# Performance work log

Hardware: AMD Instinct MI355X
Metric: run time of the kernel (lower is better)

## Reference

```python
import jax, jax.numpy as jnp
import numpy as np

UNITS = 512

def gru_cell(x, h, W, U, b):
    # Keras GRUCell, reset_after=True (v2 / cuDNN-compatible formulation)
    # x: [B, D], h: [B, U], W: [D, 3U], U: [U, 3U], b: [2, 3U]
    bi, br = b[0], b[1]
    xg = x @ W + bi          # input gates  [B, 3U]
    hg = h @ U + br          # recurrent gates [B, 3U]
    xz, xr, xh = jnp.split(xg, 3, axis=-1)
    hz, hr, hh = jnp.split(hg, 3, axis=-1)
    z = jax.nn.sigmoid(xz + hz)
    r = jax.nn.sigmoid(xr + hr)
    cand = jnp.tanh(xh + r * hh)
    return z * h + (1.0 - z) * cand

def setup_inputs() -> dict:
    key = jax.random.key(0)
    ks = jax.random.split(key, 7)
    B, T, D, U = 64, 1024, 512, UNITS
    s_in = 1.0 / np.sqrt(D)
    s_rec = 1.0 / np.sqrt(U)
    return {
        "x":  jax.random.normal(ks[0], (B, T, D), dtype=jnp.float32),
        "W0": jax.random.normal(ks[1], (D, 3 * U), dtype=jnp.float32) * s_in,
        "U0": jax.random.normal(ks[2], (U, 3 * U), dtype=jnp.float32) * s_rec,
        "b0": jax.random.normal(ks[3], (2, 3 * U), dtype=jnp.float32) * 0.01,
        "W1": jax.random.normal(ks[4], (U, 3 * U), dtype=jnp.float32) * s_rec,
        "U1": jax.random.normal(ks[5], (U, 3 * U), dtype=jnp.float32) * s_rec,
        "b1": jax.random.normal(ks[6], (2, 3 * U), dtype=jnp.float32) * 0.01,
    }

def reference(x, W0, U0, b0, W1, U1, b1):
    B = x.shape[0]
    h0_init = jnp.zeros((B, UNITS), dtype=x.dtype)
    h1_init = jnp.zeros((B, UNITS), dtype=x.dtype)

    def step(carry, x_t):
        h0, h1 = carry
        h0 = gru_cell(x_t, h0, W0, U0, b0)   # cell 0 consumes input
        h1 = gru_cell(h0, h1, W1, U1, b1)    # cell 1 consumes cell 0 output
        return (h0, h1), None

    xs = jnp.swapaxes(x, 0, 1)  # [T, B, D] for scan over time
    (h0, h1), _ = jax.lax.scan(step, (h0_init, h1_init), xs)
    # RNN(return_sequences=False) returns last-step output of last cell
    return h1
```

## Files before the change

kernel.cpp:

```cpp
#include <hip/hip_runtime.h>


typedef __bf16 bf16x8 __attribute__((ext_vector_type(8)));
typedef float  f32x4  __attribute__((ext_vector_type(4)));
typedef unsigned int uint4v __attribute__((ext_vector_type(4)));

#define T_STEPS 1024
#define NWG 256
#define NTHR 256
#define SMEM_BYTES (98304 + 4096 + 1024 + 128 + 16)

__device__ __align__(16) unsigned int g_h0[1025LL * 64 * 512];
__device__ __align__(16) unsigned int g_h1[1025LL * 64 * 512];
__device__ unsigned int g_leaf[8 * 64];
__device__ unsigned int g_root[64];
__device__ unsigned int g_epoch[64];
__device__ __align__(256) unsigned int g_flag[2][2][8][64];

__device__ __forceinline__ void f2hilo(float f, unsigned short& hi, unsigned short& lo) {
    __bf16 h = (__bf16)f;
    float  fh = (float)h;
    __bf16 l = (__bf16)(f - fh);
    hi = __builtin_bit_cast(unsigned short, h);
    lo = __builtin_bit_cast(unsigned short, l);
}

__device__ __forceinline__ f32x4 mfma16(bf16x8 a, bf16x8 b, f32x4 c) {
    return __builtin_amdgcn_mfma_f32_16x16x32_bf16(a, b, c, 0, 0, 0);
}

__device__ __forceinline__ void unpack8(const unsigned int* p, bf16x8& ah, bf16x8& al) {
    uint4v v0 = *(const uint4v*)p;
    uint4v v1 = *(const uint4v*)(p + 4);
    uint4v h, l;
    h.x = __builtin_amdgcn_perm(v0.y, v0.x, 0x07060302u);
    h.y = __builtin_amdgcn_perm(v0.w, v0.z, 0x07060302u);
    h.z = __builtin_amdgcn_perm(v1.y, v1.x, 0x07060302u);
    h.w = __builtin_amdgcn_perm(v1.w, v1.z, 0x07060302u);
    l.x = __builtin_amdgcn_perm(v0.y, v0.x, 0x05040100u);
    l.y = __builtin_amdgcn_perm(v0.w, v0.z, 0x05040100u);
    l.z = __builtin_amdgcn_perm(v1.y, v1.x, 0x05040100u);
    l.w = __builtin_amdgcn_perm(v1.w, v1.z, 0x05040100u);
    ah = __builtin_bit_cast(bf16x8, h);
    al = __builtin_bit_cast(bf16x8, l);
}

__device__ __forceinline__ void cvt8(const float* p, bf16x8& ah, bf16x8& al) {
    float4 a = *(const float4*)p;
    float4 b = *(const float4*)(p + 4);
    float f[8] = {a.x, a.y, a.z, a.w, b.x, b.y, b.z, b.w};
    bf16x8 h, l;
    #pragma unroll
    for (int i = 0; i < 8; ++i) {
        __bf16 hv = (__bf16)f[i];
        h[i] = hv;
        l[i] = (__bf16)(f[i] - (float)hv);
    }
    ah = h; al = l;
}

__device__ __forceinline__ void gemm_pass(
    bool useX, int pass, int ntile, int lane, int lcol, int kch,
    const float* A0x, const unsigned int* Ap,
    const unsigned short* sBhi, const unsigned short* sBlo,
    f32x4& acc_zr, f32x4& acc_xh, f32x4& acc_hh)
{
    bf16x8 bzero = {};
    if (ntile == 0) {
        #pragma unroll 4
        for (int ks = 0; ks < 16; ++ks) {
            bf16x8 ah, al;
            if (useX) cvt8(A0x + ks * 32 + kch * 8, ah, al);
            else      unpack8(Ap + ks * 32 + kch * 8, ah, al);
            const int o = pass * 12288 + ks * 512 + lane * 8;
            bf16x8 bh = *(const bf16x8*)(sBhi + o);
            bf16x8 bl = *(const bf16x8*)(sBlo + o);
            acc_zr = mfma16(ah, bh, acc_zr);
            acc_zr = mfma16(ah, bl, acc_zr);
            acc_zr = mfma16(al, bh, acc_zr);
        }
    } else {
        #pragma unroll 4
        for (int ks = 0; ks < 16; ++ks) {
            bf16x8 ah, al;
            if (useX) cvt8(A0x + ks * 32 + kch * 8, ah, al);
            else      unpack8(Ap + ks * 32 + kch * 8, ah, al);
            bf16x8 bh = bzero, bl = bzero;
            if (lcol < 8) {
                const int e = kch * 8 + lcol;
                const int o = pass * 12288 + 8192 + ks * 256 + e * 8;
                bh = *(const bf16x8*)(sBhi + o);
                bl = *(const bf16x8*)(sBlo + o);
            }
            f32x4 acc = pass ? acc_hh : acc_xh;
            acc = mfma16(ah, bh, acc);
            acc = mfma16(ah, bl, acc);
            acc = mfma16(al, bh, acc);
            if (pass) acc_hh = acc; else acc_xh = acc;
        }
    }
}

__device__ __forceinline__ float epilogue_hn(
    int tid, int mtile, int ntile, int lane, int lcol,
    const f32x4& acc_zr, const f32x4& acc_xh, const f32x4& acc_hh,
    float* sAcc, float* sHprev, const float* sBias)
{
    const int drow = mtile * 16 + (lane >> 4) * 4;
    if (ntile == 0) {
        #pragma unroll
        for (int r2 = 0; r2 < 4; ++r2) sAcc[(drow + r2) * 16 + lcol] = acc_zr[r2];
    } else if (lcol < 8) {
        #pragma unroll
        for (int r2 = 0; r2 < 4; ++r2) {
            sAcc[512 + (drow + r2) * 8 + lcol] = acc_xh[r2];
            sAcc[768 + (drow + r2) * 8 + lcol] = acc_hh[r2];
        }
    }
    __syncthreads();
    const int ml  = tid >> 3;
    const int col = tid & 7;
    const float zp = sAcc[ml * 16 + col]     + sBias[col];
    const float rp = sAcc[ml * 16 + 8 + col] + sBias[8 + col];
    const float z = 1.f / (1.f + __expf(-zp));
    const float r = 1.f / (1.f + __expf(-rp));
    const float xh = sAcc[512 + ml * 8 + col] + sBias[16 + col];
    const float hh = sAcc[768 + ml * 8 + col] + sBias[24 + col];
    const float ct = tanhf(xh + r * hh);
    const float hp = sHprev[tid];
    const float hn = z * hp + (1.f - z) * ct;
    sHprev[tid] = hn;
    return hn;
}

__device__ __forceinline__ void wait_one(const unsigned int* P, unsigned int target, int tid) {
    if (tid < 64) {
        while (true) {
            unsigned int v = __hip_atomic_load(P + tid, __ATOMIC_RELAXED,
                                               __HIP_MEMORY_SCOPE_AGENT);
            if (__ballot(v >= target) == ~0ull) break;
            __builtin_amdgcn_s_sleep(1);
        }
    }
    __syncthreads();
}

__device__ __forceinline__ void wait_two(const unsigned int* Pa, unsigned int ta,
                                         const unsigned int* Pb, unsigned int tb, int tid) {
    if (tid < 64) {
        bool da = false, db = false;
        while (true) {
            if (!da) {
                unsigned int v = __hip_atomic_load(Pa + tid, __ATOMIC_RELAXED,
                                                   __HIP_MEMORY_SCOPE_AGENT);
                da = (__ballot(v >= ta) == ~0ull);
            }
            if (!db) {
                unsigned int v = __hip_atomic_load(Pb + tid, __ATOMIC_RELAXED,
                                                   __HIP_MEMORY_SCOPE_AGENT);
                db = (__ballot(v >= tb) == ~0ull);
            }
            if (da && db) break;
            __builtin_amdgcn_s_sleep(1);
        }
    }
    __syncthreads();
}

__global__ void __launch_bounds__(NTHR, 1) gru_persistent(
    const float* __restrict__ x,  const float* __restrict__ W0,
    const float* __restrict__ U0, const float* __restrict__ b0,
    const float* __restrict__ W1, const float* __restrict__ U1,
    const float* __restrict__ b1, float* __restrict__ out)
{
    extern __shared__ char smem[];
    unsigned short* sBhi = (unsigned short*)smem;
    unsigned short* sBlo = sBhi + 24576;
    float* sAcc   = (float*)(smem + 98304);
    float* sHprev = sAcc + 1024;
    float* sBias  = sHprev + 256;
    unsigned int* sE0 = (unsigned int*)(sBias + 32);

    const int wg    = blockIdx.x;
    const int g     = wg >> 7;
    const int cell  = (wg >> 6) & 1;
    const int slice = wg & 63;
    const int c0    = slice * 8;
    const int tid   = threadIdx.x;

    __builtin_amdgcn_fence(__ATOMIC_ACQUIRE, "agent");

    if (tid == 0)
        sE0[0] = __hip_atomic_load(&g_epoch[0], __ATOMIC_RELAXED, __HIP_MEMORY_SCOPE_AGENT);

    {
        const int ml = tid >> 3, col = tid & 7;
        unsigned int* dst = (cell ? g_h1 : g_h0)
                          + (long long)(g * 32 + ml) * 512 + (c0 + col);
        __hip_atomic_store(dst, 0u, __ATOMIC_RELAXED, __HIP_MEMORY_SCOPE_AGENT);
    }
    if (tid < 8) {
        unsigned int* f = &g_flag[0][0][0][0];
        __hip_atomic_store(f + wg * 8 + tid, 0u, __ATOMIC_RELAXED, __HIP_MEMORY_SCOPE_AGENT);
    }

    {
        const float* Wm = cell ? W1 : W0;
        const float* Um = cell ? U1 : U0;
        for (int e = tid; e < 24576; e += NTHR) {
            const int pass = e / 12288;
            const int rem  = e % 12288;
            int j, gcol;
            if (rem < 8192) {
                const int ks = rem >> 9, r2 = rem & 511;
                const int entry = r2 >> 3, i = r2 & 7;
                const int col = entry & 15, kch = entry >> 4;
                j = ks * 32 + kch * 8 + i;
                gcol = (col < 8) ? (c0 + col) : (512 + c0 + col - 8);
            } else {
                const int r2 = rem - 8192;
                const int ks = r2 >> 8, r3 = r2 & 255;
                const int entry = r3 >> 3, i = r3 & 7;
                const int col = entry & 7, kch = entry >> 3;
                j = ks * 32 + kch * 8 + i;
                gcol = 1024 + c0 + col;
            }
            const float v = (pass ? Um : Wm)[j * 1536 + gcol];
            f2hilo(v, sBhi[e], sBlo[e]);
        }
    }
    {
        const float* b = cell ? b1 : b0;
        if (tid < 32) {
            const int col = tid & 7, sec = tid >> 3;
            float v;
            if (sec == 0)      v = b[c0 + col] + b[1536 + c0 + col];
            else if (sec == 1) v = b[512 + c0 + col] + b[1536 + 512 + c0 + col];
            else if (sec == 2) v = b[1024 + c0 + col];
            else               v = b[1536 + 1024 + c0 + col];
            sBias[tid] = v;
        }
        sHprev[tid] = 0.f;
    }
    __syncthreads();
    const unsigned int E0 = sE0[0];

    {
        const unsigned int target = E0 + 1u;
        if (tid == 0) {
            asm volatile("s_waitcnt vmcnt(0)" ::: "memory");
            unsigned int o = __hip_atomic_fetch_add(&g_leaf[(wg & 7) * 64], 1u,
                                __ATOMIC_RELAXED, __HIP_MEMORY_SCOPE_AGENT);
            if (o == 32u * target - 1u) {
                unsigned int r = __hip_atomic_fetch_add(&g_root[0], 1u,
                                    __ATOMIC_RELAXED, __HIP_MEMORY_SCOPE_AGENT);
                if (r == 8u * target - 1u)
                    __hip_atomic_store(&g_epoch[0], target,
                                       __ATOMIC_RELAXED, __HIP_MEMORY_SCOPE_AGENT);
            }
        }
        while ((int)(__hip_atomic_load(&g_epoch[0], __ATOMIC_RELAXED,
                                       __HIP_MEMORY_SCOPE_AGENT) - target) < 0)
            __builtin_amdgcn_s_sleep(1);
        asm volatile("" ::: "memory");
        __syncthreads();
    }

    const int lane  = tid & 63;
    const int mtile = (tid >> 6) & 1;
    const int ntile = tid >> 7;
    const int lcol  = lane & 15;
    const int kch   = lane >> 4;
    const int arow  = g * 32 + mtile * 16 + lcol;

    if (cell == 0) {
        unsigned int* const myflag = &g_flag[0][g][0][0];
        for (int k = 0; k < T_STEPS; ++k) {
            f32x4 acc_zr = {0.f, 0.f, 0.f, 0.f};
            f32x4 acc_xh = {0.f, 0.f, 0.f, 0.f};
            f32x4 acc_hh = {0.f, 0.f, 0.f, 0.f};
            const float* A0x = x + ((long long)arow * 1024 + k) * 512;
            gemm_pass(true, 0, ntile, lane, lcol, kch, A0x, nullptr,
                      sBhi, sBlo, acc_zr, acc_xh, acc_hh);

            if (k > 0)
                wait_one(&g_flag[0][g][(k - 1) & 7][0], (unsigned int)k, tid);

            const unsigned int* A1p = g_h0 + ((long long)k * (64 * 512)) + arow * 512;
            gemm_pass(false, 1, ntile, lane, lcol, kch, nullptr, A1p,
                      sBhi, sBlo, acc_zr, acc_xh, acc_hh);

            const float hn = epilogue_hn(tid, mtile, ntile, lane, lcol,
                                         acc_zr, acc_xh, acc_hh, sAcc, sHprev, sBias);
            {
                const int ml = tid >> 3, col = tid & 7;
                unsigned short hi_, lo_;
                f2hilo(hn, hi_, lo_);
                const unsigned int pk = ((unsigned int)hi_ << 16) | (unsigned int)lo_;
                unsigned int* dst = g_h0 + (long long)(k + 1) * (64 * 512)
                                  + (long long)(g * 32 + ml) * 512 + (c0 + col);
                __hip_atomic_store(dst, pk, __ATOMIC_RELAXED, __HIP_MEMORY_SCOPE_AGENT);
            }
            __syncthreads();
            if (tid == 0)
                __hip_atomic_store(myflag + ((k & 7) * 64) + slice, (unsigned int)(k + 1),
                                   __ATOMIC_RELAXED, __HIP_MEMORY_SCOPE_AGENT);
        }
    } else {
        unsigned int* const myflag = &g_flag[1][g][0][0];
        for (int t = 0; t < T_STEPS; ++t) {
            if (t > 0)
                wait_two(&g_flag[1][g][(t - 1) & 7][0], (unsigned int)t,
                         &g_flag[0][g][t & 7][0], (unsigned int)(t + 1), tid);
            else
                wait_one(&g_flag[0][g][0][0], 1u, tid);

            f32x4 acc_zr = {0.f, 0.f, 0.f, 0.f};
            f32x4 acc_xh = {0.f, 0.f, 0.f, 0.f};
            f32x4 acc_hh = {0.f, 0.f, 0.f, 0.f};
            const unsigned int* A0p = g_h0 + ((long long)(t + 1) * (64 * 512)) + arow * 512;
            const unsigned int* A1p = g_h1 + ((long long)t * (64 * 512)) + arow * 512;
            gemm_pass(false, 0, ntile, lane, lcol, kch, nullptr, A0p,
                      sBhi, sBlo, acc_zr, acc_xh, acc_hh);
            gemm_pass(false, 1, ntile, lane, lcol, kch, nullptr, A1p,
                      sBhi, sBlo, acc_zr, acc_xh, acc_hh);

            const float hn = epilogue_hn(tid, mtile, ntile, lane, lcol,
                                         acc_zr, acc_xh, acc_hh, sAcc, sHprev, sBias);
            {
                const int ml = tid >> 3, col = tid & 7;
                unsigned short hi_, lo_;
                f2hilo(hn, hi_, lo_);
                const unsigned int pk = ((unsigned int)hi_ << 16) | (unsigned int)lo_;
                unsigned int* dst = g_h1 + (long long)(t + 1) * (64 * 512)
                                  + (long long)(g * 32 + ml) * 512 + (c0 + col);
                __hip_atomic_store(dst, pk, __ATOMIC_RELAXED, __HIP_MEMORY_SCOPE_AGENT);
                if (t == T_STEPS - 1)
                    out[(g * 32 + ml) * 512 + (c0 + col)] = hn;
            }
            __syncthreads();
            if (tid == 0)
                __hip_atomic_store(myflag + ((t & 7) * 64) + slice, (unsigned int)(t + 1),
                                   __ATOMIC_RELAXED, __HIP_MEMORY_SCOPE_AGENT);
        }
    }
}

extern "C" void kernel_launch(void* const* d_in, const int* in_sizes, int n_in,
                              void* d_out, int out_size, void* d_ws, size_t ws_size,
                              hipStream_t stream) {
    (void)in_sizes; (void)n_in; (void)d_ws; (void)ws_size; (void)out_size;
    const float* x  = (const float*)d_in[0];
    const float* W0 = (const float*)d_in[1];
    const float* U0 = (const float*)d_in[2];
    const float* b0 = (const float*)d_in[3];
    const float* W1 = (const float*)d_in[4];
    const float* U1 = (const float*)d_in[5];
    const float* b1 = (const float*)d_in[6];
    float* out = (float*)d_out;

    hipFuncSetAttribute((const void*)gru_persistent,
                        hipFuncAttributeMaxDynamicSharedMemorySize, SMEM_BYTES);
    void* args[] = {&x, &W0, &U0, &b0, &W1, &U1, &b1, &out};
    hipLaunchCooperativeKernel((const void*)gru_persistent, dim3(NWG), dim3(NTHR),
                               args, SMEM_BYTES, stream);
}
```

Before: 10.70 ms.

## Replace per-slice flag polling with monotonic counters and overlap cell1 recurrent GEMM

Each slice used to publish its own step flag in a ring buffer, and waiters polled all 64 flags with a wavefront ballot. Now each slice does one atomic increment on a shared per-group counter per step, and one thread polls a single word with sleep backoff. Counters are never reset; each launch reads them at startup and uses that value as its baseline. Cell 1 now runs its recurrent GEMM on its own previous state before waiting on cell 0's current output, so that work overlaps with cell 0, at the cost of 64-way atomic contention on one address.

```diff
diff --git a/kernel.cpp b/kernel.cpp
--- a/kernel.cpp
+++ b/kernel.cpp
@@ -8,14 +8,15 @@
 #define T_STEPS 1024
 #define NWG 256
 #define NTHR 256
-#define SMEM_BYTES (98304 + 4096 + 1024 + 128 + 16)
+#define SMEM_BYTES (98304 + 4096 + 1024 + 128 + 32)
 
 __device__ __align__(16) unsigned int g_h0[1025LL * 64 * 512];
 __device__ __align__(16) unsigned int g_h1[1025LL * 64 * 512];
 __device__ unsigned int g_leaf[8 * 64];
 __device__ unsigned int g_root[64];
 __device__ unsigned int g_epoch[64];
-__device__ __align__(256) unsigned int g_flag[2][2][8][64];
+__device__ __align__(256) unsigned int g_cnt[2][2][64];
+__device__ __align__(256) unsigned int g_cntx[2][64];
 
 __device__ __forceinline__ void f2hilo(float f, unsigned short& hi, unsigned short& lo) {
     __bf16 h = (__bf16)f;
@@ -133,35 +134,14 @@
     return hn;
 }
 
-__device__ __forceinline__ void wait_one(const unsigned int* P, unsigned int target, int tid) {
-    if (tid < 64) {
-        while (true) {
-            unsigned int v = __hip_atomic_load(P + tid, __ATOMIC_RELAXED,
-                                               __HIP_MEMORY_SCOPE_AGENT);
-            if (__ballot(v >= target) == ~0ull) break;
-            __builtin_amdgcn_s_sleep(1);
-        }
-    }
-    __syncthreads();
-}
-
-__device__ __forceinline__ void wait_two(const unsigned int* Pa, unsigned int ta,
-                                         const unsigned int* Pb, unsigned int tb, int tid) {
-    if (tid < 64) {
-        bool da = false, db = false;
-        while (true) {
-            if (!da) {
-                unsigned int v = __hip_atomic_load(Pa + tid, __ATOMIC_RELAXED,
-                                                   __HIP_MEMORY_SCOPE_AGENT);
-                da = (__ballot(v >= ta) == ~0ull);
-            }
-            if (!db) {
-                unsigned int v = __hip_atomic_load(Pb + tid, __ATOMIC_RELAXED,
-                                                   __HIP_MEMORY_SCOPE_AGENT);
-                db = (__ballot(v >= tb) == ~0ull);
-            }
-            if (da && db) break;
-            __builtin_amdgcn_s_sleep(1);
+__device__ __forceinline__ void wait_cnt(unsigned int* C, unsigned int target, int tid) {
+    if (tid == 0) {
+        int spins = 0;
+        while ((int)(__hip_atomic_load(C, __ATOMIC_RELAXED,
+                                       __HIP_MEMORY_SCOPE_AGENT) - target) < 0) {
+            if (spins < 4) __builtin_amdgcn_s_sleep(1);
+            else           __builtin_amdgcn_s_sleep(8);
+            ++spins;
         }
     }
     __syncthreads();
@@ -190,18 +170,17 @@
 
     __builtin_amdgcn_fence(__ATOMIC_ACQUIRE, "agent");
 
-    if (tid == 0)
+    if (tid == 0) {
         sE0[0] = __hip_atomic_load(&g_epoch[0], __ATOMIC_RELAXED, __HIP_MEMORY_SCOPE_AGENT);
+        sE0[1] = __hip_atomic_load(&g_cnt[cell][g][0], __ATOMIC_RELAXED, __HIP_MEMORY_SCOPE_AGENT);
+        sE0[2] = __hip_atomic_load(&g_cntx[g][0], __ATOMIC_RELAXED, __HIP_MEMORY_SCOPE_AGENT);
+    }
 
     {
         const int ml = tid >> 3, col = tid & 7;
         unsigned int* dst = (cell ? g_h1 : g_h0)
                           + (long long)(g * 32 + ml) * 512 + (c0 + col);
         __hip_atomic_store(dst, 0u, __ATOMIC_RELAXED, __HIP_MEMORY_SCOPE_AGENT);
-    }
-    if (tid < 8) {
-        unsigned int* f = &g_flag[0][0][0][0];
-        __hip_atomic_store(f + wg * 8 + tid, 0u, __ATOMIC_RELAXED, __HIP_MEMORY_SCOPE_AGENT);
     }
 
     {
@@ -243,7 +222,9 @@
         sHprev[tid] = 0.f;
     }
     __syncthreads();
-    const unsigned int E0 = sE0[0];
+    const unsigned int E0     = sE0[0];
+    const unsigned int Cown   = sE0[1];
+    const unsigned int Ccross = sE0[2];
 
     {
         const unsigned int target = E0 + 1u;
@@ -272,9 +253,12 @@
     const int lcol  = lane & 15;
     const int kch   = lane >> 4;
     const int arow  = g * 32 + mtile * 16 + lcol;
+    const int ml    = tid >> 3;
+    const int colw  = tid & 7;
 
     if (cell == 0) {
-        unsigned int* const myflag = &g_flag[0][g][0][0];
+        unsigned int* const cnt  = &g_cnt[0][g][0];
+        unsigned int* const cntx = &g_cntx[g][0];
         for (int k = 0; k < T_STEPS; ++k) {
             f32x4 acc_zr = {0.f, 0.f, 0.f, 0.f};
             f32x4 acc_xh = {0.f, 0.f, 0.f, 0.f};
@@ -283,8 +267,7 @@
             gemm_pass(true, 0, ntile, lane, lcol, kch, A0x, nullptr,
                       sBhi, sBlo, acc_zr, acc_xh, acc_hh);
 
-            if (k > 0)
-                wait_one(&g_flag[0][g][(k - 1) & 7][0], (unsigned int)k, tid);
+            if (k > 0) wait_cnt(cnt, Cown + 64u * (unsigned int)k, tid);
 
             const unsigned int* A1p = g_h0 + ((long long)k * (64 * 512)) + arow * 512;
             gemm_pass(false, 1, ntile, lane, lcol, kch, nullptr, A1p,
@@ -293,55 +276,54 @@
             const float hn = epilogue_hn(tid, mtile, ntile, lane, lcol,
                                          acc_zr, acc_xh, acc_hh, sAcc, sHprev, sBias);
             {
-                const int ml = tid >> 3, col = tid & 7;
                 unsigned short hi_, lo_;
                 f2hilo(hn, hi_, lo_);
                 const unsigned int pk = ((unsigned int)hi_ << 16) | (unsigned int)lo_;
                 unsigned int* dst = g_h0 + (long long)(k + 1) * (64 * 512)
-                                  + (long long)(g * 32 + ml) * 512 + (c0 + col);
+                                  + (long long)(g * 32 + ml) * 512 + (c0 + colw);
                 __hip_atomic_store(dst, pk, __ATOMIC_RELAXED, __HIP_MEMORY_SCOPE_AGENT);
             }
             __syncthreads();
-            if (tid == 0)
-                __hip_atomic_store(myflag + ((k & 7) * 64) + slice, (unsigned int)(k + 1),
-                                   __ATOMIC_RELAXED, __HIP_MEMORY_SCOPE_AGENT);
+            if (tid == 0) {
+                __hip_atomic_fetch_add(cnt, 1u, __ATOMIC_RELAXED, __HIP_MEMORY_SCOPE_AGENT);
+                __hip_atomic_fetch_add(cntx, 1u, __ATOMIC_RELAXED, __HIP_MEMORY_SCOPE_AGENT);
+            }
         }
     } else {
-        unsigned int* const myflag = &g_flag[1][g][0][0];
+        unsigned int* const cnt   = &g_cnt[1][g][0];
+        unsigned int* const cntUp = &g_cntx[g][0];
         for (int t = 0; t < T_STEPS; ++t) {
-            if (t > 0)
-                wait_two(&g_flag[1][g][(t - 1) & 7][0], (unsigned int)t,
-                         &g_flag[0][g][t & 7][0], (unsigned int)(t + 1), tid);
-            else
-                wait_one(&g_flag[0][g][0][0], 1u, tid);
+            if (t > 0) wait_cnt(cnt, Cown + 64u * (unsigned int)t, tid);
 
             f32x4 acc_zr = {0.f, 0.f, 0.f, 0.f};
             f32x4 acc_xh = {0.f, 0.f, 0.f, 0.f};
             f32x4 acc_hh = {0.f, 0.f, 0.f, 0.f};
+
+            const unsigned int* A1p = g_h1 + ((long long)t * (64 * 512)) + arow * 512;
+            gemm_pass(false, 1, ntile, lane, lcol, kch, nullptr, A1p,
+                      sBhi, sBlo, acc_zr, acc_xh, acc_hh);
+
+            wait_cnt(cntUp, Ccross + 64u * (unsigned int)(t + 1), tid);
+
             const unsigned int* A0p = g_h0 + ((long long)(t + 1) * (64 * 512)) + arow * 512;
-            const unsigned int* A1p = g_h1 + ((long long)t * (64 * 512)) + arow * 512;
             gemm_pass(false, 0, ntile, lane, lcol, kch, nullptr, A0p,
-                      sBhi, sBlo, acc_zr, acc_xh, acc_hh);
-            gemm_pass(false, 1, ntile, lane, lcol, kch, nullptr, A1p,
                       sBhi, sBlo, acc_zr, acc_xh, acc_hh);
 
             const float hn = epilogue_hn(tid, mtile, ntile, lane, lcol,
                                          acc_zr, acc_xh, acc_hh, sAcc, sHprev, sBias);
             {
-                const int ml = tid >> 3, col = tid & 7;
                 unsigned short hi_, lo_;
                 f2hilo(hn, hi_, lo_);
                 const unsigned int pk = ((unsigned int)hi_ << 16) | (unsigned int)lo_;
                 unsigned int* dst = g_h1 + (long long)(t + 1) * (64 * 512)
-                                  + (long long)(g * 32 + ml) * 512 + (c0 + col);
+                                  + (long long)(g * 32 + ml) * 512 + (c0 + colw);
                 __hip_atomic_store(dst, pk, __ATOMIC_RELAXED, __HIP_MEMORY_SCOPE_AGENT);
                 if (t == T_STEPS - 1)
-                    out[(g * 32 + ml) * 512 + (c0 + col)] = hn;
+                    out[(g * 32 + ml) * 512 + (c0 + colw)] = hn;
             }
             __syncthreads();
             if (tid == 0)
-                __hip_atomic_store(myflag + ((t & 7) * 64) + slice, (unsigned int)(t + 1),
-                                   __ATOMIC_RELAXED, __HIP_MEMORY_SCOPE_AGENT);
+                __hip_atomic_fetch_add(cnt, 1u, __ATOMIC_RELAXED, __HIP_MEMORY_SCOPE_AGENT);
         }
     }
 }
@@ -359,9 +341,14 @@
     const float* b1 = (const float*)d_in[6];
     float* out = (float*)d_out;
 
-    hipFuncSetAttribute((const void*)gru_persistent,
-                        hipFuncAttributeMaxDynamicSharedMemorySize, SMEM_BYTES);
+    (void)hipFuncSetAttribute((const void*)gru_persistent,
+                              hipFuncAttributeMaxDynamicSharedMemorySize, SMEM_BYTES);
     void* args[] = {&x, &W0, &U0, &b0, &W1, &U1, &b1, &out};
-    hipLaunchCooperativeKernel((const void*)gru_persistent, dim3(NWG), dim3(NTHR),
-                               args, SMEM_BYTES, stream);
-}
+    hipError_t e = hipLaunchCooperativeKernel((const void*)gru_persistent,
+                                              dim3(NWG), dim3(NTHR),
+                                              args, SMEM_BYTES, stream);
+    if (e != hipSuccess) {
+        gru_persistent<<<dim3(NWG), dim3(NTHR), SMEM_BYTES, stream>>>(
+            x, W0, U0, b0, W1, U1, b1, out);
+    }
+}
```

New measurement: 9.999 ms. 6.6% less time.
